# Optimization experiments

Hardware: AMD Instinct MI355X
Metric: run time of the kernel (lower is better)

Reference implementation:

```python
import jax, jax.numpy as jnp
import numpy as np

N_NODES = 100000
N_EDGES = 1200000
K1, K2 = 4096, 256  # TopKPooling ratios (int ratio => absolute k in PyG)
NEG_SLOPE = 0.01    # nn.LeakyReLU default


def leaky(v):
    return jnp.where(v >= 0, v, NEG_SLOPE * v)


def gcn_conv(x, src, dst, w, W, b):
    """PyG GCNConv: x @ W, symmetric-normalized aggregation with self-loops, + bias.
    Removed edges are represented by weight 0 (identical math to edge removal)."""
    N = x.shape[0]
    x = x @ W                                            # [N, out]
    deg = jax.ops.segment_sum(w, dst, num_segments=N) + 1.0  # +1 self-loop
    dinv = jax.lax.rsqrt(deg)
    norm = dinv[src] * w * dinv[dst]                     # per-edge norm
    agg = jax.ops.segment_sum(x[src] * norm[:, None], dst, num_segments=N)
    agg = agg + x * (dinv * dinv)[:, None]               # self-loop term
    return agg + b


def topk_pool(x, src, dst, w, p, k):
    """PyG TopKPooling: score = tanh(x.p/||p||), keep top-k, scale by score,
    relabel edges; dropped edges get weight 0 (mapped to node 0 harmlessly)."""
    N = x.shape[0]
    score = jnp.tanh((x @ p) / jnp.linalg.norm(p))
    top_scores, perm = jax.lax.top_k(score, k)
    x_new = x[perm] * top_scores[:, None]
    mapping = jnp.zeros(N, jnp.int32).at[perm].set(jnp.arange(k, dtype=jnp.int32))
    kept = jnp.zeros(N, dtype=bool).at[perm].set(True)
    valid = kept[src] & kept[dst]
    return x_new, mapping[src], mapping[dst], jnp.where(valid, w, 0.0)


def setup_inputs() -> dict:
    key = jax.random.key(0)
    ks = jax.random.split(key, 12)
    pos = jax.random.normal(ks[0], (N_NODES, 3), dtype=jnp.float32)
    edge_index = jax.random.randint(ks[1], (2, N_EDGES), 0, N_NODES, dtype=jnp.int64)

    def glorot(k, shape):
        lim = np.sqrt(6.0 / (shape[0] + shape[-1]))
        return jax.random.uniform(k, shape, jnp.float32, -lim, lim)

    return {
        "pos": pos,
        "edge_index": edge_index,
        "W1": glorot(ks[2], (3, 64)),    "b1": jnp.zeros((64,), jnp.float32),
        "W2": glorot(ks[3], (64, 128)),  "b2": jnp.zeros((128,), jnp.float32),
        "W3": glorot(ks[4], (128, 256)), "b3": jnp.zeros((256,), jnp.float32),
        "p1": jax.random.normal(ks[5], (64,), jnp.float32),
        "p2": jax.random.normal(ks[6], (256,), jnp.float32),
        "fcW": glorot(ks[7], (256 * 256, 512)),
        "fcb": jnp.zeros((512,), jnp.float32),
    }


def reference(pos, edge_index, W1, b1, W2, b2, W3, b3, p1, p2, fcW, fcb):
    src, dst = edge_index[0], edge_index[1]
    w = jnp.ones(src.shape[0], dtype=pos.dtype)

    x = leaky(gcn_conv(pos, src, dst, w, W1, b1))          # [N, 64]
    x, src, dst, w = topk_pool(x, src, dst, w, p1, K1)     # [4096, 64]
    x = leaky(gcn_conv(x, src, dst, w, W2, b2))            # [4096, 128]
    x = leaky(gcn_conv(x, src, dst, w, W3, b3))            # [4096, 256]
    x, src, dst, w = topk_pool(x, src, dst, w, p2, K2)     # [256, 256]

    x = x.T.reshape(-1)                                    # transpose(0,1) + flatten
    return x @ fcW + fcb                                   # [512]
```

## Files before the change

kernel.cpp:

```cpp
#include <hip/hip_runtime.h>
#include <cstdint>
#include <cstddef>

#define NNODES 100000
#define NEDGES 1200000
#define KP1 4096
#define KP2 256
#define CAP_CAND 16384
#define CAP1 48
#define CAP2 48
#define NSAMP 2048
#define TAURANK 167
#define NXCD 8
#define DRANGE 12500

typedef unsigned long long u64;
typedef unsigned int u32;

__device__ __forceinline__ double leakyd(double v){ return v >= 0.0 ? v : 0.01*v; }

__device__ __forceinline__ u64 mono64(double d){
  u64 b = (u64)__double_as_longlong(d);
  return (b & 0x8000000000000000ull) ? ~b : (b | 0x8000000000000000ull);
}

__device__ __forceinline__ void get_edge(const int* eb, int flag, int e, int& s, int& d){
  if (flag){ s = eb[2*e]; d = eb[2*(NEDGES+e)]; }
  else     { s = eb[e];   d = eb[NEDGES+e]; }
}

__global__ void k_meta(const int* eb, const float* p1, const float* p2, int* meta, double* dscal){
  __shared__ double red[256];
  int t = threadIdx.x;
  double s1 = 0.0;
  if (t < 64){ double v = (double)p1[t]; s1 = v*v; }
  red[t] = s1; __syncthreads();
  for (int w = 128; w > 0; w >>= 1){ if (t < w) red[t] += red[t+w]; __syncthreads(); }
  if (t == 0) dscal[0] = 1.0 / sqrt(red[0]);
  __syncthreads();
  double v2 = (double)p2[t];
  red[t] = v2*v2; __syncthreads();
  for (int w = 128; w > 0; w >>= 1){ if (t < w) red[t] += red[t+w]; __syncthreads(); }
  if (t == 0){
    dscal[1] = 1.0 / sqrt(red[0]);
    int is64 = 1;
    for (int i = 1; i <= 127; i += 2) if (eb[i] != 0){ is64 = 0; break; }
    meta[0] = is64;
  }
}

__global__ __launch_bounds__(256) void k_scatter(const int* eb, const int* meta, int* cnt1, int* csrf){
  int e = (blockIdx.x >> 3)*256 + threadIdx.x;
  int x = blockIdx.x & 7;
  if (e >= NEDGES) return;
  int s, d; get_edge(eb, meta[0], e, s, d);
  if (d/DRANGE != x) return;
  int slot = atomicAdd(&cnt1[d], 1);
  if (slot < CAP1) csrf[(size_t)d*CAP1 + slot] = s;
}

__global__ void k_prep(const int* cnt1, const float* pos, double4* posw){
  int n = blockIdx.x*256 + threadIdx.x;
  if (n >= NNODES) return;
  double di = 1.0 / sqrt((double)cnt1[n] + 1.0);
  double4 v;
  v.x = (double)pos[3*n+0]*di;
  v.y = (double)pos[3*n+1]*di;
  v.z = (double)pos[3*n+2]*di;
  v.w = di;
  posw[n] = v;
}

__global__ __launch_bounds__(256) void k_score1(const int* cnt1, const int* csrf,
                         const double4* posw,
                         const float* W1, const float* b1, const float* p1,
                         double* score1raw, u64* key1){
  int gid = blockIdx.x*256 + threadIdx.x;
  int n = gid >> 2;
  int l = gid & 3;
  if (n >= NNODES) return;
  int c = cnt1[n]; if (c > CAP1) c = CAP1;
  const int4* row = (const int4*)(csrf + (size_t)n*CAP1);
  int4 r0 = row[l];
  int4 r1 = make_int4(0,0,0,0);
  int4 r2 = make_int4(0,0,0,0);
  if (c > 16) r1 = row[l+4];
  if (c > 32) r2 = row[l+8];
  double t0 = 0.0, t1 = 0.0, t2 = 0.0;
  auto g = [&](int sidx, bool liv){
    if (liv){
      double4 p = posw[sidx];
      t0 += p.x; t1 += p.y; t2 += p.z;
    }
  };
  int j0 = l*4;
  g(r0.x, j0+0 < c); g(r0.y, j0+1 < c); g(r0.z, j0+2 < c); g(r0.w, j0+3 < c);
  int j1 = l*4 + 16;
  g(r1.x, j1+0 < c); g(r1.y, j1+1 < c); g(r1.z, j1+2 < c); g(r1.w, j1+3 < c);
  int j2 = l*4 + 32;
  g(r2.x, j2+0 < c); g(r2.y, j2+1 < c); g(r2.z, j2+2 < c); g(r2.w, j2+3 < c);
  for (int o = 1; o < 4; o <<= 1){
    t0 += __shfl_xor(t0, o, 64);
    t1 += __shfl_xor(t1, o, 64);
    t2 += __shfl_xor(t2, o, 64);
  }
  double4 pwn = posw[n];
  double di = pwn.w;
  t0 = (t0 + pwn.x)*di;
  t1 = (t1 + pwn.y)*di;
  t2 = (t2 + pwn.z)*di;
  double acc = 0.0;
  #pragma unroll
  for (int f16 = 0; f16 < 16; ++f16){
    int f = l*16 + f16;
    double h = t0*(double)W1[f] + t1*(double)W1[64+f] + t2*(double)W1[128+f] + (double)b1[f];
    acc += leakyd(h) * (double)p1[f];
  }
  acc += __shfl_xor(acc, 1, 64);
  acc += __shfl_xor(acc, 2, 64);
  if (l == 0){
    score1raw[n] = acc;
    key1[n] = (mono64(acc) & ~0x1FFFFull) | (u64)(131071 - n);
  }
}

__global__ __launch_bounds__(256) void k_tau(const u64* key1, u64* tau){
  __shared__ u64 smp[NSAMP];
  int t = threadIdx.x;
  int sid = blockIdx.x*256 + t;
  for (int i = t; i < NSAMP; i += 256) smp[i] = key1[(size_t)i*48];
  __syncthreads();
  u64 mykey = smp[sid];
  int rank = 0;
  for (int j = 0; j < NSAMP; ++j) rank += (smp[j] > mykey) ? 1 : 0;
  if (rank == TAURANK) tau[0] = mykey;
}

__global__ void k_collect(const u64* key1, const u64* tau, int* cand, u64* candkey, int* cnt){
  int n = blockIdx.x*256 + threadIdx.x;
  if (n >= NNODES) return;
  u64 k = key1[n];
  if (k >= tau[0]){
    int p = atomicAdd(&cnt[0], 1);
    if (p < CAP_CAND){ cand[p] = n; candkey[p] = k; }
  }
}

__global__ __launch_bounds__(256) void k_rankA(const u64* candkey, const int* cnt, int* rank){
  int C = cnt[0]; if (C > CAP_CAND) C = CAP_CAND;
  int ci = blockIdx.x, kj = blockIdx.y;
  if (ci*256 >= C || kj*256 >= C) return;
  __shared__ u64 tile[256];
  int t = threadIdx.x;
  int kidx = kj*256 + t;
  tile[t] = (kidx < C) ? candkey[kidx] : 0ull;
  __syncthreads();
  int idx = ci*256 + t;
  if (idx >= C) return;
  u64 mykey = candkey[idx];
  int r = 0;
  #pragma unroll 8
  for (int j = 0; j < 256; ++j) r += (tile[j] > mykey) ? 1 : 0;
  if (r) atomicAdd(&rank[idx], r);
}

__global__ void k_rankB(const int* cand, const int* cnt, const int* rank,
                        int* perm1, int* mapping){
  int idx = blockIdx.x*256 + threadIdx.x;
  int C = cnt[0]; if (C > CAP_CAND) C = CAP_CAND;
  if (idx >= C) return;
  int r = rank[idx];
  if (r < KP1){
    int node = cand[idx];
    perm1[r] = node;
    mapping[node] = r;
  }
}

__global__ __launch_bounds__(256) void k_pool1(const int* perm1, const int* cnt1, const int* csrf,
                          const int* mapping, const double4* posw, const double* score1raw,
                          const float* W1, const float* b1, const double* dscal,
                          int* csr2, int* deg2, double* dinv2, double* x1p){
  int r = blockIdx.x*4 + (threadIdx.x >> 6);
  int l = threadIdx.x & 63;
  int n = perm1[r];
  int c = cnt1[n]; if (c > CAP1) c = CAP1;
  int srcn = -1;
  if (l < c) srcn = csrf[(size_t)n*CAP1 + l];
  int m = -1;
  if (srcn >= 0) m = mapping[srcn];
  u64 bal = __ballot(m >= 0);
  int pre = __popcll(bal & ((1ull << l) - 1ull));
  if (m >= 0 && pre < CAP2) csr2[r*CAP2 + pre] = m;
  if (l == 0){
    int k = __popcll(bal); if (k > CAP2) k = CAP2;
    deg2[r] = k;
    dinv2[r] = 1.0 / sqrt((double)k + 1.0);
  }
  double t0 = 0.0, t1 = 0.0, t2 = 0.0;
  if (l < c){
    double4 p = posw[srcn];
    t0 = p.x; t1 = p.y; t2 = p.z;
  }
  #pragma unroll
  for (int o = 1; o < 64; o <<= 1){
    t0 += __shfl_xor(t0, o, 64);
    t1 += __shfl_xor(t1, o, 64);
    t2 += __shfl_xor(t2, o, 64);
  }
  double4 pwn = posw[n];
  double di = pwn.w;
  t0 = (t0 + pwn.x)*di;
  t1 = (t1 + pwn.y)*di;
  t2 = (t2 + pwn.z)*di;
  double sc = tanh(score1raw[n] * dscal[0]);
  double h = t0*(double)W1[l] + t1*(double)W1[64+l] + t2*(double)W1[128+l] + (double)b1[l];
  x1p[r*64+l] = leakyd(h) * sc;
}

__global__ __launch_bounds__(128) void k_x2(const int* csr2, const int* deg2, const double* dinv2,
                                            const double* x1p, const float* W2, const float* b2, double* x2){
  __shared__ double xin[64];
  int r = blockIdx.x, t = threadIdx.x;
  double dr = dinv2[r];
  if (t < 64){
    double a = 0.0;
    int c = deg2[r];
    for (int j = 0; j < c; ++j){
      int s = csr2[r*CAP2+j];
      a += x1p[s*64+t]*dinv2[s];
    }
    xin[t] = a*dr + x1p[r*64+t]*dr*dr;
  }
  __syncthreads();
  double acc = 0.0;
  for (int c = 0; c < 64; ++c) acc += xin[c]*(double)W2[c*128+t];
  x2[r*128+t] = leakyd(acc + (double)b2[t]);
}

__global__ __launch_bounds__(256) void k_x3(const int* csr2, const int* deg2, const double* dinv2,
                                            const double* x2, const float* W3, const float* b3,
                                            const float* p2, const double* dscal,
                                            double* x3, double* score2, u64* key2){
  __shared__ double xin[128];
  __shared__ double red[256];
  int r = blockIdx.x, t = threadIdx.x;
  double dr = dinv2[r];
  if (t < 128){
    double a = 0.0;
    int c = deg2[r];
    for (int j = 0; j < c; ++j){
      int s = csr2[r*CAP2+j];
      a += x2[s*128+t]*dinv2[s];
    }
    xin[t] = a*dr + x2[r*128+t]*dr*dr;
  }
  __syncthreads();
  double acc = 0.0;
  for (int c = 0; c < 128; ++c) acc += xin[c]*(double)W3[c*256+t];
  double val = leakyd(acc + (double)b3[t]);
  x3[r*256+t] = val;
  red[t] = val * (double)p2[t];
  __syncthreads();
  for (int w = 128; w > 0; w >>= 1){ if (t < w) red[t] += red[t+w]; __syncthreads(); }
  if (t == 0){
    score2[r] = tanh(red[0] * dscal[1]);
    key2[r] = (mono64(red[0]) & ~0x1FFFFull) | (u64)(131071 - r);
  }
}

__global__ __launch_bounds__(256) void k_rank2A(const u64* key2, int* rank2){
  __shared__ u64 tile[256];
  int t = threadIdx.x;
  tile[t] = key2[blockIdx.y*256 + t];
  __syncthreads();
  int idx = blockIdx.x*256 + t;
  u64 mykey = key2[idx];
  int r = 0;
  #pragma unroll 8
  for (int j = 0; j < 256; ++j) r += (tile[j] > mykey) ? 1 : 0;
  if (r) atomicAdd(&rank2[idx], r);
}

__global__ void k_rank2B(const int* rank2, const double* score2, int* perm2, double* sc2){
  int idx = blockIdx.x*256 + threadIdx.x;
  int r = rank2[idx];
  if (r < KP2){
    perm2[r] = idx;
    sc2[r] = score2[idx];
  }
}

__global__ __launch_bounds__(512) void k_fc(const double* x3, const int* perm2, const double* sc2,
                                            const float* fcW, double* partial){
  __shared__ double xs[128];
  int b = blockIdx.x, t = threadIdx.x;
  if (t < 128){
    int f = b >> 1;
    int n = ((b & 1) << 7) + t;
    xs[t] = x3[(size_t)perm2[n]*256 + f] * sc2[n];
  }
  __syncthreads();
  const float* Wp = fcW + (size_t)b*128*512 + t;
  double acc = 0.0;
  #pragma unroll 8
  for (int i = 0; i < 128; ++i) acc += xs[i]*(double)Wp[(size_t)i*512];
  partial[b*512+t] = acc;
}

__global__ __launch_bounds__(128) void k_out(const double* partial, const float* fcb, float* out){
  __shared__ double red[128];
  int o = blockIdx.x, t = threadIdx.x;
  double a = 0.0;
  for (int b = t; b < 512; b += 128) a += partial[(size_t)b*512+o];
  red[t] = a; __syncthreads();
  for (int w = 64; w > 0; w >>= 1){ if (t < w) red[t] += red[t+w]; __syncthreads(); }
  if (t == 0) out[o] = (float)(red[0] + (double)fcb[o]);
}

extern "C" void kernel_launch(void* const* d_in, const int* in_sizes, int n_in,
                              void* d_out, int out_size, void* d_ws, size_t ws_size,
                              hipStream_t stream){
  const float* pos = (const float*)d_in[0];
  const int*   eb  = (const int*)d_in[1];
  const float* W1  = (const float*)d_in[2];
  const float* b1  = (const float*)d_in[3];
  const float* W2  = (const float*)d_in[4];
  const float* b2  = (const float*)d_in[5];
  const float* W3  = (const float*)d_in[6];
  const float* b3  = (const float*)d_in[7];
  const float* p1  = (const float*)d_in[8];
  const float* p2  = (const float*)d_in[9];
  const float* fcW = (const float*)d_in[10];
  const float* fcb = (const float*)d_in[11];
  float* out = (float*)d_out;

  char* w = (char*)d_ws;
  size_t off = 0;
  auto alloc = [&](size_t bytes)->char*{
    char* p = w + off; off = (off + bytes + 255) & ~(size_t)255; return p;
  };
  int*   cnt1   = (int*)  alloc((size_t)NNODES*4);
  int*   cnt    = (int*)  alloc(64*4);
  int*   rank1  = (int*)  alloc(CAP_CAND*4);
  int*   rank2  = (int*)  alloc(KP1*4);
  size_t zero_bytes = off;
  int*   mapping= (int*)  alloc((size_t)NNODES*4);
  int*    meta  = (int*)  alloc(64*4);
  double* dscal = (double*)alloc(8*8);
  u64*   tau    = (u64*)  alloc(8*8);
  double4* posw = (double4*)alloc((size_t)NNODES*32);
  double* score1= (double*)alloc((size_t)NNODES*8);
  u64*   key1   = (u64*)  alloc((size_t)NNODES*8);
  int*   cand   = (int*)  alloc(CAP_CAND*4);
  u64*   candkey= (u64*)  alloc(CAP_CAND*8);
  int*   perm1  = (int*)  alloc(KP1*4);
  double* x1p   = (double*)alloc((size_t)KP1*64*8);
  int*   csr2   = (int*)  alloc((size_t)KP1*CAP2*4);
  int*   deg2   = (int*)  alloc(KP1*4);
  double* dinv2 = (double*)alloc(KP1*8);
  char*  csrf_base = alloc((size_t)NNODES*CAP1*4);
  int*   csrf   = (int*)csrf_base;
  size_t aoff = 0;
  auto alloc2 = [&](size_t bytes)->char*{
    char* p = csrf_base + aoff; aoff = (aoff + bytes + 255) & ~(size_t)255; return p;
  };
  double* x2    = (double*)alloc2((size_t)KP1*128*8);
  double* x3    = (double*)alloc2((size_t)KP1*256*8);
  double* score2= (double*)alloc2(KP1*8);
  u64*   key2   = (u64*)  alloc2(KP1*8);
  int*   perm2  = (int*)  alloc2(KP2*4);
  double* sc2   = (double*)alloc2(KP2*8);
  double* partial=(double*)alloc2((size_t)512*512*8);
  if (off > ws_size) return;

  hipMemsetAsync(d_ws, 0, zero_bytes, stream);
  hipMemsetAsync(mapping, 0xFF, (size_t)NNODES*4, stream);

  k_meta<<<1,256,0,stream>>>(eb, p1, p2, meta, dscal);
  k_scatter<<<((NEDGES+255)/256)*NXCD,256,0,stream>>>(eb, meta, cnt1, csrf);
  k_prep<<<(NNODES+255)/256,256,0,stream>>>(cnt1, pos, posw);
  k_score1<<<(NNODES*4+255)/256,256,0,stream>>>(cnt1, csrf, posw, W1, b1, p1,
                                                score1, key1);
  k_tau<<<NSAMP/256,256,0,stream>>>(key1, tau);
  k_collect<<<(NNODES+255)/256,256,0,stream>>>(key1, tau, cand, candkey, cnt);
  {
    dim3 g(CAP_CAND/256, CAP_CAND/256);
    k_rankA<<<g,256,0,stream>>>(candkey, cnt, rank1);
  }
  k_rankB<<<CAP_CAND/256,256,0,stream>>>(cand, cnt, rank1, perm1, mapping);
  k_pool1<<<KP1/4,256,0,stream>>>(perm1, cnt1, csrf, mapping, posw, score1, W1, b1, dscal,
                                  csr2, deg2, dinv2, x1p);
  k_x2<<<KP1,128,0,stream>>>(csr2, deg2, dinv2, x1p, W2, b2, x2);
  k_x3<<<KP1,256,0,stream>>>(csr2, deg2, dinv2, x2, W3, b3, p2, dscal, x3, score2, key2);
  {
    dim3 g(KP1/256, KP1/256);
    k_rank2A<<<g,256,0,stream>>>(key2, rank2);
  }
  k_rank2B<<<KP1/256,256,0,stream>>>(rank2, score2, perm2, sc2);
  k_fc<<<512,512,0,stream>>>(x3, perm2, sc2, fcW, partial);
  k_out<<<512,128,0,stream>>>(partial, fcb, out);
}
```

Baseline: 218.8 us.

## Fold workspace initialization into kernels and merge second-pool rank kernels

Removes the separate 0xFF memset for the mapping array and the zeroing of cnt/rank1/rank2. That initialization now happens inside k_meta and k_collect, so the zeroing memset only covers cnt1. The two-kernel, atomic-based rank computation for the second top-k is replaced by a single kernel in which each block loads all 4096 keys into shared memory and counts rank directly. This cuts launch count and atomics, but gives the rank pass only 16 blocks doing 4096 comparisons per thread.

```diff
diff --git a/kernel.cpp b/kernel.cpp
--- a/kernel.cpp
+++ b/kernel.cpp
@@ -29,9 +29,11 @@
   else     { s = eb[e];   d = eb[NEDGES+e]; }
 }
 
-__global__ void k_meta(const int* eb, const float* p1, const float* p2, int* meta, double* dscal){
+__global__ void k_meta(const int* eb, const float* p1, const float* p2, int* meta, double* dscal,
+                       int* cnt){
   __shared__ double red[256];
   int t = threadIdx.x;
+  if (t < 64) cnt[t] = 0;
   double s1 = 0.0;
   if (t < 64){ double v = (double)p1[t]; s1 = v*v; }
   red[t] = s1; __syncthreads();
@@ -136,9 +138,12 @@
   if (rank == TAURANK) tau[0] = mykey;
 }
 
-__global__ void k_collect(const u64* key1, const u64* tau, int* cand, u64* candkey, int* cnt){
+__global__ void k_collect(const u64* key1, const u64* tau, int* cand, u64* candkey, int* cnt,
+                          int* mapping, int* rank1){
   int n = blockIdx.x*256 + threadIdx.x;
   if (n >= NNODES) return;
+  mapping[n] = -1;
+  if (n < CAP_CAND) rank1[n] = 0;
   u64 k = key1[n];
   if (k >= tau[0]){
     int p = atomicAdd(&cnt[0], 1);
@@ -269,22 +274,17 @@
   }
 }
 
-__global__ __launch_bounds__(256) void k_rank2A(const u64* key2, int* rank2){
-  __shared__ u64 tile[256];
+__global__ __launch_bounds__(256) void k_rank2(const u64* key2, const double* score2,
+                                               int* perm2, double* sc2){
+  __shared__ u64 keys[KP1];
   int t = threadIdx.x;
-  tile[t] = key2[blockIdx.y*256 + t];
+  for (int i = t; i < KP1; i += 256) keys[i] = key2[i];
   __syncthreads();
   int idx = blockIdx.x*256 + t;
-  u64 mykey = key2[idx];
+  u64 mykey = keys[idx];
   int r = 0;
   #pragma unroll 8
-  for (int j = 0; j < 256; ++j) r += (tile[j] > mykey) ? 1 : 0;
-  if (r) atomicAdd(&rank2[idx], r);
-}
-
-__global__ void k_rank2B(const int* rank2, const double* score2, int* perm2, double* sc2){
-  int idx = blockIdx.x*256 + threadIdx.x;
-  int r = rank2[idx];
+  for (int j = 0; j < KP1; ++j) r += (keys[j] > mykey) ? 1 : 0;
   if (r < KP2){
     perm2[r] = idx;
     sc2[r] = score2[idx];
@@ -341,10 +341,9 @@
     char* p = w + off; off = (off + bytes + 255) & ~(size_t)255; return p;
   };
   int*   cnt1   = (int*)  alloc((size_t)NNODES*4);
+  size_t zero_bytes = off;
   int*   cnt    = (int*)  alloc(64*4);
   int*   rank1  = (int*)  alloc(CAP_CAND*4);
-  int*   rank2  = (int*)  alloc(KP1*4);
-  size_t zero_bytes = off;
   int*   mapping= (int*)  alloc((size_t)NNODES*4);
   int*    meta  = (int*)  alloc(64*4);
   double* dscal = (double*)alloc(8*8);
@@ -375,15 +374,14 @@
   if (off > ws_size) return;
 
   hipMemsetAsync(d_ws, 0, zero_bytes, stream);
-  hipMemsetAsync(mapping, 0xFF, (size_t)NNODES*4, stream);
-
-  k_meta<<<1,256,0,stream>>>(eb, p1, p2, meta, dscal);
+
+  k_meta<<<1,256,0,stream>>>(eb, p1, p2, meta, dscal, cnt);
   k_scatter<<<((NEDGES+255)/256)*NXCD,256,0,stream>>>(eb, meta, cnt1, csrf);
   k_prep<<<(NNODES+255)/256,256,0,stream>>>(cnt1, pos, posw);
   k_score1<<<(NNODES*4+255)/256,256,0,stream>>>(cnt1, csrf, posw, W1, b1, p1,
                                                 score1, key1);
   k_tau<<<NSAMP/256,256,0,stream>>>(key1, tau);
-  k_collect<<<(NNODES+255)/256,256,0,stream>>>(key1, tau, cand, candkey, cnt);
+  k_collect<<<(NNODES+255)/256,256,0,stream>>>(key1, tau, cand, candkey, cnt, mapping, rank1);
   {
     dim3 g(CAP_CAND/256, CAP_CAND/256);
     k_rankA<<<g,256,0,stream>>>(candkey, cnt, rank1);
@@ -393,11 +391,7 @@
                                   csr2, deg2, dinv2, x1p);
   k_x2<<<KP1,128,0,stream>>>(csr2, deg2, dinv2, x1p, W2, b2, x2);
   k_x3<<<KP1,256,0,stream>>>(csr2, deg2, dinv2, x2, W3, b3, p2, dscal, x3, score2, key2);
-  {
-    dim3 g(KP1/256, KP1/256);
-    k_rank2A<<<g,256,0,stream>>>(key2, rank2);
-  }
-  k_rank2B<<<KP1/256,256,0,stream>>>(rank2, score2, perm2, sc2);
+  k_rank2<<<KP1/256,256,0,stream>>>(key2, score2, perm2, sc2);
   k_fc<<<512,512,0,stream>>>(x3, perm2, sc2, fcW, partial);
   k_out<<<512,128,0,stream>>>(partial, fcb, out);
 }
```

New measurement: 270.2 us. 1.23x slower.
